# Kernel tuning notes

Measured on AMD Instinct MI355X. Metric: run time of the kernel, lower is better.

The kernel has to match this reference:

```python
import jax, jax.numpy as jnp
import numpy as np

B, C, H, W = 128, 768, 14, 14
D = 128          # d_graph
K = 8            # top_k
LN_EPS = 1e-5
NORM_EPS = 1e-12


def setup_inputs() -> dict:
    key = jax.random.key(0)
    ks = jax.random.split(key, 12)
    s = lambda k, shape, fan: jax.random.normal(k, shape, jnp.float32) / np.sqrt(fan)
    return {
        "feat_map": jax.random.normal(ks[0], (B, C, H, W), jnp.float32),
        # node_proj: Linear(C, D) + LayerNorm(D)
        "W_node": s(ks[1], (C, D), C), "b_node": jnp.zeros((D,), jnp.float32),
        "ln_g": jnp.ones((D,), jnp.float32), "ln_b": jnp.zeros((D,), jnp.float32),
        # pos_mlp: Linear(2, 64) -> GELU -> Linear(64, D)
        "Wp1": s(ks[2], (2, 64), 2), "bp1": jnp.zeros((64,), jnp.float32),
        "Wp2": s(ks[3], (64, D), 64), "bp2": jnp.zeros((D,), jnp.float32),
        # edge_mlp: Linear(3D, D) -> GELU -> Linear(D, D)
        "We1": s(ks[4], (3 * D, D), 3 * D), "be1": jnp.zeros((D,), jnp.float32),
        "We2": s(ks[5], (D, D), D), "be2": jnp.zeros((D,), jnp.float32),
    }


def _layernorm(x, g, b):
    mu = jnp.mean(x, axis=-1, keepdims=True)
    var = jnp.mean(jnp.square(x - mu), axis=-1, keepdims=True)
    return (x - mu) * jax.lax.rsqrt(var + LN_EPS) * g + b


def reference(feat_map, W_node, b_node, ln_g, ln_b, Wp1, bp1, Wp2, bp2, We1, be1, We2, be2):
    Bm, Cm, Hm, Wm = feat_map.shape
    N = Hm * Wm
    tokens = feat_map.reshape(Bm, Cm, N).transpose(0, 2, 1)            # [B,N,C]
    nodes = jax.nn.gelu(_layernorm(tokens @ W_node + b_node, ln_g, ln_b), approximate=False)  # [B,N,D]

    ys = jnp.linspace(0.0, 1.0, Hm)
    xs = jnp.linspace(0.0, 1.0, Wm)
    gy, gx = jnp.meshgrid(ys, xs, indexing='ij')
    coords = jnp.stack([gy.reshape(-1), gx.reshape(-1)], axis=-1)       # [N,2]
    coords = jnp.broadcast_to(coords[None], (Bm, N, 2))

    nrm = nodes / jnp.maximum(jnp.linalg.norm(nodes, axis=-1, keepdims=True), NORM_EPS)
    sim = jnp.einsum('bnd,bmd->bnm', nrm, nrm)
    sim = sim - jnp.eye(N, dtype=sim.dtype)[None] * 1e9
    _, adj = jax.lax.top_k(sim, K)                                      # [B,N,K]

    adj_flat = adj.reshape(Bm, N * K, 1)
    neighbor_nodes = jnp.take_along_axis(nodes, adj_flat, axis=1).reshape(Bm, N, K, -1)
    neighbor_coords = jnp.take_along_axis(coords, adj_flat, axis=1).reshape(Bm, N, K, 2)

    disp = neighbor_coords - coords[:, :, None, :]                      # [B,N,K,2]
    spatial_feat = jax.nn.gelu(disp @ Wp1 + bp1, approximate=False) @ Wp2 + bp2  # [B,N,K,D]

    source = jnp.broadcast_to(nodes[:, :, None, :], neighbor_nodes.shape)
    edge_input = jnp.concatenate([source, neighbor_nodes, spatial_feat], axis=-1)  # [B,N,K,3D]
    edges = jax.nn.gelu(edge_input @ We1 + be1, approximate=False) @ We2 + be2
    return nodes, edges, adj
```

## Files before the change

kernel.cpp:

```cpp
#include <hip/hip_runtime.h>

#define BB 128
#define CC 768
#define NN 196
#define DD 128
#define KTOP 8
#define MROWS 25088

typedef unsigned short u16;
typedef unsigned int u32;

typedef __attribute__((ext_vector_type(8))) short bf16x8;
typedef __attribute__((ext_vector_type(4))) float f32x4;

__device__ __forceinline__ u16 f2bfu(float x) {
    u32 i; __builtin_memcpy(&i, &x, 4);
    u32 r = (i + 0x7fffu + ((i >> 16) & 1u)) >> 16;
    return (u16)r;
}
__device__ __forceinline__ float bfu2f(u16 h) {
    u32 x = ((u32)h) << 16; float f; __builtin_memcpy(&f, &x, 4); return f;
}
__device__ __forceinline__ float gelu_f(float x) {
    return 0.5f * x * (1.0f + erff(x * 0.70710678118654752f));
}

__global__ __launch_bounds__(256)
void pack_we1_kernel(const float* __restrict__ We1, uint4* __restrict__ WPH,
                     uint4* __restrict__ WPL)
{
    const int eid = blockIdx.x * 256 + threadIdx.x;
    const int mat = eid >> 11, rem = eid & 2047;
    const int kc = rem >> 9, ct = (rem >> 6) & 7, l = rem & 63;
    const int g = l >> 4, c = ct * 16 + (l & 15);
    const int krow = mat * 128 + kc * 32 + g * 8;
    u32 h[4], lo[4];
#pragma unroll
    for (int jp = 0; jp < 4; ++jp) {
        const float w0 = We1[(size_t)(krow + 2 * jp) * DD + c];
        const float w1 = We1[(size_t)(krow + 2 * jp + 1) * DD + c];
        const u16 h0 = f2bfu(w0), h1 = f2bfu(w1);
        const u16 l0 = f2bfu(w0 - bfu2f(h0)), l1 = f2bfu(w1 - bfu2f(h1));
        h[jp]  = (u32)h0 | ((u32)h1 << 16);
        lo[jp] = (u32)l0 | ((u32)l1 << 16);
    }
    WPH[eid] = make_uint4(h[0], h[1], h[2], h[3]);
    WPL[eid] = make_uint4(lo[0], lo[1], lo[2], lo[3]);
}

__global__ __launch_bounds__(128)
void gemm_node_kernel(const float* __restrict__ feat, const float* __restrict__ Wn,
                      float* __restrict__ part)
{
    __shared__ float As[32][32];
    __shared__ float Bs[32][DD];
    const int tid = threadIdx.x;
    const int m0  = blockIdx.x * 32;
    const int k0  = blockIdx.y * 384;

    const int r_ld   = tid & 31;
    const int cl_ld  = tid >> 5;
    const int m_ld   = m0 + r_ld;
    const int b_ld   = m_ld / NN;
    const int n_ld   = m_ld % NN;
    const float* fbase = feat + (size_t)b_ld * CC * NN + n_ld;

    const int rg = tid >> 5;
    const int cg = tid & 31;

    float acc[8][4];
#pragma unroll
    for (int i = 0; i < 8; ++i)
#pragma unroll
        for (int j = 0; j < 4; ++j) acc[i][j] = 0.0f;

    for (int kt = 0; kt < 12; ++kt) {
        const int kbase = k0 + kt * 32;
#pragma unroll
        for (int p = 0; p < 8; ++p) {
            const int cl = cl_ld + 4 * p;
            As[cl][r_ld] = fbase[(size_t)(kbase + cl) * NN];
        }
#pragma unroll
        for (int p = 0; p < 8; ++p) {
            const int q = tid + 128 * p;
            const int cl = q >> 5, d4 = (q & 31) * 4;
            *(float4*)(&Bs[cl][d4]) = *(const float4*)(&Wn[(size_t)(kbase + cl) * DD + d4]);
        }
        __syncthreads();
#pragma unroll
        for (int kk = 0; kk < 32; ++kk) {
            const float4 a0 = *(const float4*)(&As[kk][rg * 8]);
            const float4 a1 = *(const float4*)(&As[kk][rg * 8 + 4]);
            const float4 bv = *(const float4*)(&Bs[kk][cg * 4]);
            const float af[8] = {a0.x, a0.y, a0.z, a0.w, a1.x, a1.y, a1.z, a1.w};
#pragma unroll
            for (int i = 0; i < 8; ++i) {
                acc[i][0] += af[i] * bv.x; acc[i][1] += af[i] * bv.y;
                acc[i][2] += af[i] * bv.z; acc[i][3] += af[i] * bv.w;
            }
        }
        __syncthreads();
    }
    float* op = part + ((size_t)blockIdx.y * MROWS + m0 + rg * 8) * DD + cg * 4;
#pragma unroll
    for (int i = 0; i < 8; ++i) {
        *(float4*)(op + (size_t)i * DD) =
            make_float4(acc[i][0], acc[i][1], acc[i][2], acc[i][3]);
    }
}

__global__ __launch_bounds__(128)
void ln_kernel(const float* __restrict__ part, const float* __restrict__ bnode,
               const float* __restrict__ lng, const float* __restrict__ lnb,
               float* __restrict__ nodes, float* __restrict__ inv_norm)
{
    __shared__ float vals[8][DD];
    __shared__ float stats[8][2];
    const int tid = threadIdx.x;
    const int row0 = blockIdx.x * 8;
    const int d = tid;
    const float bb = bnode[d];
#pragma unroll
    for (int r = 0; r < 8; ++r) {
        const size_t m = row0 + r;
        vals[r][d] = part[m * DD + d] + part[(size_t)(MROWS + m) * DD + d] + bb;
    }
    __syncthreads();
    const int lane = tid & 63, wv = tid >> 6;
    for (int r = wv * 4; r < wv * 4 + 4; ++r) {
        float a0 = vals[r][lane], a1 = vals[r][lane + 64];
        float s = a0 + a1;
#pragma unroll
        for (int off = 32; off > 0; off >>= 1) s += __shfl_xor(s, off);
        const float mu = s * (1.0f / 128.0f);
        float d0 = a0 - mu, d1 = a1 - mu;
        float s2 = d0 * d0 + d1 * d1;
#pragma unroll
        for (int off = 32; off > 0; off >>= 1) s2 += __shfl_xor(s2, off);
        if (lane == 0) { stats[r][0] = mu; stats[r][1] = rsqrtf(s2 * (1.0f/128.0f) + 1e-5f); }
    }
    __syncthreads();
    const float g  = lng[d];
    const float be = lnb[d];
    float acc[8];
#pragma unroll
    for (int r = 0; r < 8; ++r) {
        const float y = (vals[r][d] - stats[r][0]) * stats[r][1] * g + be;
        acc[r] = gelu_f(y);
    }
    __syncthreads();
#pragma unroll
    for (int r = 0; r < 8; ++r) vals[r][d] = acc[r] * acc[r];
#pragma unroll
    for (int r = 0; r < 8; ++r) nodes[(size_t)(row0 + r) * DD + d] = acc[r];
    __syncthreads();
    for (int r = wv * 4; r < wv * 4 + 4; ++r) {
        float s = vals[r][lane] + vals[r][lane + 64];
#pragma unroll
        for (int off = 32; off > 0; off >>= 1) s += __shfl_xor(s, off);
        if (lane == 0) inv_norm[row0 + r] = 1.0f / fmaxf(sqrtf(s), 1e-12f);
    }
}

__global__ __launch_bounds__(256)
void s1n1_kernel(const float* __restrict__ nodes, const uint4* __restrict__ WPH,
                 const uint4* __restrict__ WPL, float* __restrict__ S1,
                 float* __restrict__ N1)
{
    __shared__ uint4 AfH[4][4][64];
    __shared__ uint4 AfL[4][4][64];
    const int tid = threadIdx.x;
    const int m0 = blockIdx.x * 64;

#pragma unroll
    for (int p = 0; p < 8; ++p) {
        const int idx = tid + 256 * p;
        const int r = idx >> 5, d0 = (idx & 31) * 4;
        const float4 v = *(const float4*)(&nodes[(size_t)(m0 + r) * DD + d0]);
        const u16 h0 = f2bfu(v.x), h1 = f2bfu(v.y), h2 = f2bfu(v.z), h3 = f2bfu(v.w);
        const u16 l0 = f2bfu(v.x - bfu2f(h0)), l1 = f2bfu(v.y - bfu2f(h1));
        const u16 l2 = f2bfu(v.z - bfu2f(h2)), l3 = f2bfu(v.w - bfu2f(h3));
        const int rt = r >> 4, kc = d0 >> 5;
        const int ln = (((d0 >> 3) & 3) << 4) | (r & 15);
        const int half = (d0 >> 2) & 1;
        u32* ph = (u32*)&AfH[rt][kc][ln];
        u32* pl = (u32*)&AfL[rt][kc][ln];
        ph[half * 2]     = (u32)h0 | ((u32)h1 << 16);
        ph[half * 2 + 1] = (u32)h2 | ((u32)h3 << 16);
        pl[half * 2]     = (u32)l0 | ((u32)l1 << 16);
        pl[half * 2 + 1] = (u32)l2 | ((u32)l3 << 16);
    }
    __syncthreads();

    const int l  = tid & 63;
    const int wv = tid >> 6;
    const int wr = wv >> 1, wc = wv & 1;

    f32x4 acc[2][8];
#pragma unroll
    for (int rt = 0; rt < 2; ++rt)
#pragma unroll
        for (int ct = 0; ct < 8; ++ct) {
            f32x4 z = {0.0f, 0.0f, 0.0f, 0.0f};
            acc[rt][ct] = z;
        }

#pragma unroll
    for (int kc = 0; kc < 4; ++kc) {
        bf16x8 aH[2], aL[2];
#pragma unroll
        for (int rt = 0; rt < 2; ++rt) {
            const uint4 uh = AfH[wr * 2 + rt][kc][l];
            const uint4 ul = AfL[wr * 2 + rt][kc][l];
            __builtin_memcpy(&aH[rt], &uh, 16);
            __builtin_memcpy(&aL[rt], &ul, 16);
        }
#pragma unroll
        for (int ct = 0; ct < 8; ++ct) {
            const uint4 uh = WPH[((wc * 4 + kc) * 8 + ct) * 64 + l];
            const uint4 ul = WPL[((wc * 4 + kc) * 8 + ct) * 64 + l];
            bf16x8 bH, bL;
            __builtin_memcpy(&bH, &uh, 16);
            __builtin_memcpy(&bL, &ul, 16);
#pragma unroll
            for (int rt = 0; rt < 2; ++rt) {
                acc[rt][ct] = __builtin_amdgcn_mfma_f32_16x16x32_bf16(aH[rt], bH, acc[rt][ct], 0, 0, 0);
                acc[rt][ct] = __builtin_amdgcn_mfma_f32_16x16x32_bf16(aL[rt], bH, acc[rt][ct], 0, 0, 0);
                acc[rt][ct] = __builtin_amdgcn_mfma_f32_16x16x32_bf16(aH[rt], bL, acc[rt][ct], 0, 0, 0);
            }
        }
    }

    float* outb = wc ? N1 : S1;
    const int cl  = l & 15;
    const int rq0 = (l >> 4) * 4;
#pragma unroll
    for (int rt = 0; rt < 2; ++rt)
#pragma unroll
        for (int q = 0; q < 4; ++q) {
            const size_t row = m0 + wr * 32 + rt * 16 + rq0 + q;
#pragma unroll
            for (int ct = 0; ct < 8; ++ct)
                outb[row * DD + ct * 16 + cl] = acc[rt][ct][q];
        }
}

__global__ __launch_bounds__(256)
void sim_kernel(const float* __restrict__ nodes, const float* __restrict__ inv_norm,
                float* __restrict__ sim)
{
    __shared__ float as[28][36];
    __shared__ float bs[NN][36];
    __shared__ float invs[NN];
    const int tid = threadIdx.x;
    const int b  = blockIdx.x / 7;
    const int n0 = (blockIdx.x % 7) * 28;
    const float* nb = nodes + (size_t)b * NN * DD;
    if (tid < NN) invs[tid] = inv_norm[b * NN + tid];
    const bool act = tid < 196;
    const int ai = act ? tid / 28 : 0;
    const int bi = act ? tid % 28 : 0;
    float acc[4][7];
#pragma unroll
    for (int r = 0; r < 4; ++r)
#pragma unroll
        for (int j = 0; j < 7; ++j) acc[r][j] = 0.0f;
    for (int dc = 0; dc < DD; dc += 32) {
        __syncthreads();
        if (tid < 224) {
            const int i = tid >> 3, q = tid & 7;
            *(float4*)(&as[i][q * 4]) = *(const float4*)(&nb[(size_t)(n0 + i) * DD + dc + q * 4]);
        }
        for (int idx = tid; idx < 1568; idx += 256) {
            const int r = idx >> 3, q = idx & 7;
            *(float4*)(&bs[r][q * 4]) = *(const float4*)(&nb[(size_t)r * DD + dc + q * 4]);
        }
        __syncthreads();
        if (act) {
            for (int dd = 0; dd < 32; dd += 4) {
                float4 a4[4], b4[7];
#pragma unroll
                for (int r = 0; r < 4; ++r) a4[r] = *(const float4*)(&as[ai * 4 + r][dd]);
#pragma unroll
                for (int j = 0; j < 7; ++j) b4[j] = *(const float4*)(&bs[bi * 7 + j][dd]);
#pragma unroll
                for (int r = 0; r < 4; ++r)
#pragma unroll
                    for (int j = 0; j < 7; ++j)
                        acc[r][j] += a4[r].x * b4[j].x + a4[r].y * b4[j].y
                                   + a4[r].z * b4[j].z + a4[r].w * b4[j].w;
            }
        }
    }
    if (act) {
#pragma unroll
        for (int r = 0; r < 4; ++r) {
            const int n = n0 + ai * 4 + r;
            const float sn = invs[n];
#pragma unroll
            for (int j = 0; j < 7; ++j) {
                const int m = bi * 7 + j;
                sim[((size_t)b * NN + n) * NN + m] = acc[r][j] * sn * invs[m];
            }
        }
    }
}

__global__ __launch_bounds__(256)
void topk_kernel(const float* __restrict__ sim, int* __restrict__ adj_i,
                 float* __restrict__ adj_o, const float* __restrict__ We2,
                 uint4* __restrict__ W2P)
{
    const int bid = blockIdx.x;
    if (bid >= (BB * NN) / 4) {
        const int e  = (bid - (BB * NN) / 4) * 256 + threadIdx.x;
        const int l  = e & 63;
        const int fi = e >> 6;
        const int ks = fi >> 3, ct = fi & 7;
        const int k0 = ks * 32 + (l >> 4) * 8;
        const int c  = ct * 16 + (l & 15);
        u16 v[8];
#pragma unroll
        for (int j = 0; j < 8; ++j) v[j] = f2bfu(We2[(size_t)(k0 + j) * DD + c]);
        uint4 pk;
        pk.x = (u32)v[0] | ((u32)v[1] << 16);
        pk.y = (u32)v[2] | ((u32)v[3] << 16);
        pk.z = (u32)v[4] | ((u32)v[5] << 16);
        pk.w = (u32)v[6] | ((u32)v[7] << 16);
        W2P[e] = pk;
        return;
    }
    const int bn = bid * 4 + (threadIdx.x >> 6);
    const int n = bn % NN;
    const int lane = threadIdx.x & 63;
    const float* srow = sim + (size_t)bn * NN;
    float v[4]; int mi[4];
#pragma unroll
    for (int s = 0; s < 4; ++s) {
        const int m = lane + 64 * s;
        mi[s] = m;
        v[s] = (m < NN && m != n) ? srow[m] : -3.0e38f;
    }
    for (int r = 0; r < KTOP; ++r) {
        float bv = v[0]; int bm = mi[0];
#pragma unroll
        for (int s = 1; s < 4; ++s) { if (v[s] > bv) { bv = v[s]; bm = mi[s]; } }
#pragma unroll
        for (int off = 32; off > 0; off >>= 1) {
            const float ov = __shfl_xor(bv, off);
            const int   om = __shfl_xor(bm, off);
            if (ov > bv || (ov == bv && om < bm)) { bv = ov; bm = om; }
        }
        if (lane == 0) {
            adj_i[bn * KTOP + r] = bm;
            adj_o[bn * KTOP + r] = (float)bm;
        }
#pragma unroll
        for (int s = 0; s < 4; ++s) if (mi[s] == bm) v[s] = -3.0e38f;
    }
}

__global__ __launch_bounds__(128)
void pos_kernel(const float* __restrict__ Wp1, const float* __restrict__ bp1,
                const float* __restrict__ Wp2, const float* __restrict__ bp2,
                const float* __restrict__ We1, float* __restrict__ PC)
{
    __shared__ float t1[64];
    __shared__ float sp[DD];
    const int e = blockIdx.x;
    const int dy = e / 27 - 13, dx = e % 27 - 13;
    const float fy = (float)dy / 13.0f, fx = (float)dx / 13.0f;
    const int tid = threadIdx.x;
    if (tid < 64) {
        const float h = fy * Wp1[tid] + fx * Wp1[64 + tid] + bp1[tid];
        t1[tid] = gelu_f(h);
    }
    __syncthreads();
    float s = bp2[tid];
    for (int j = 0; j < 64; ++j) s += t1[j] * Wp2[j * DD + tid];
    sp[tid] = s;
    __syncthreads();
    float o = 0.0f;
    for (int c = 0; c < DD; ++c) o += sp[c] * We1[(size_t)(256 + c) * DD + tid];
    PC[e * DD + tid] = o;
}

__global__ __launch_bounds__(256)
void edge_kernel(const float* __restrict__ S1, const float* __restrict__ N1,
                 const float* __restrict__ PC, const int* __restrict__ adj_i,
                 const float* __restrict__ be1, const uint4* __restrict__ W2P,
                 const float* __restrict__ be2, float* __restrict__ edges_o)
{
    __shared__ uint4 ldsB[2048];
    const int tid = threadIdx.x;
    const int b  = blockIdx.x / 25;
    const int n0 = (blockIdx.x % 25) * 8;

#pragma unroll
    for (int p = 0; p < 8; ++p)
        ldsB[tid + 256 * p] = W2P[tid + 256 * p];

    const int l  = tid & 63;
    const int wv = tid >> 6;
    const int g  = l >> 4;
    const int rA = wv * 16 + (l & 15);
    const int nA0 = n0 + (rA >> 3);
    const int nA  = (nA0 < NN) ? nA0 : 0;
    const int kA  = rA & 7;
    const int m   = adj_i[((size_t)b * NN + nA) * KTOP + kA];
    const int iy = nA / 14, ix = nA % 14;
    const int my = m / 14,  mx = m % 14;
    const int di = (my - iy + 13) * 27 + (mx - ix + 13);

    const float* s1r = S1 + ((size_t)b * NN + nA) * DD;
    const float* n1r = N1 + ((size_t)b * NN + m) * DD;
    const float* pcr = PC + (size_t)di * DD;

    bf16x8 afr[4];
#pragma unroll
    for (int ks = 0; ks < 4; ++ks) {
        const int k0 = ks * 32 + g * 8;
        float u[8];
#pragma unroll
        for (int h = 0; h < 2; ++h) {
            const int k = k0 + h * 4;
            const float4 s1 = *(const float4*)(s1r + k);
            const float4 n1 = *(const float4*)(n1r + k);
            const float4 pc = *(const float4*)(pcr + k);
            const float4 b1 = *(const float4*)(be1 + k);
            u[h * 4 + 0] = gelu_f(s1.x + n1.x + pc.x + b1.x);
            u[h * 4 + 1] = gelu_f(s1.y + n1.y + pc.y + b1.y);
            u[h * 4 + 2] = gelu_f(s1.z + n1.z + pc.z + b1.z);
            u[h * 4 + 3] = gelu_f(s1.w + n1.w + pc.w + b1.w);
        }
        bf16x8 a;
#pragma unroll
        for (int j = 0; j < 8; ++j) a[j] = (short)f2bfu(u[j]);
        afr[ks] = a;
    }
    __syncthreads();

    f32x4 acc[8];
#pragma unroll
    for (int ct = 0; ct < 8; ++ct) {
        f32x4 z = {0.0f, 0.0f, 0.0f, 0.0f};
        acc[ct] = z;
    }
#pragma unroll
    for (int ks = 0; ks < 4; ++ks) {
#pragma unroll
        for (int ct = 0; ct < 8; ++ct) {
            const uint4 bw = ldsB[(ks * 8 + ct) * 64 + l];
            bf16x8 bf; __builtin_memcpy(&bf, &bw, 16);
            acc[ct] = __builtin_amdgcn_mfma_f32_16x16x32_bf16(afr[ks], bf, acc[ct], 0, 0, 0);
        }
    }

    const int cl  = l & 15;
    const int rq0 = (l >> 4) * 4;
    float be2f[8];
#pragma unroll
    for (int ct = 0; ct < 8; ++ct) be2f[ct] = be2[ct * 16 + cl];
#pragma unroll
    for (int q = 0; q < 4; ++q) {
        const int r = wv * 16 + rq0 + q;
        const int n = n0 + (r >> 3);
        if (n < NN) {
            float* op = edges_o + (((size_t)b * NN + n) * KTOP + (r & 7)) * DD;
#pragma unroll
            for (int ct = 0; ct < 8; ++ct)
                op[ct * 16 + cl] = acc[ct][q] + be2f[ct];
        }
    }
}

extern "C" void kernel_launch(void* const* d_in, const int* in_sizes, int n_in,
                              void* d_out, int out_size, void* d_ws, size_t ws_size,
                              hipStream_t stream)
{
    const float* feat = (const float*)d_in[0];
    const float* Wn   = (const float*)d_in[1];
    const float* bn   = (const float*)d_in[2];
    const float* lng  = (const float*)d_in[3];
    const float* lnb  = (const float*)d_in[4];
    const float* Wp1  = (const float*)d_in[5];
    const float* bp1  = (const float*)d_in[6];
    const float* Wp2  = (const float*)d_in[7];
    const float* bp2  = (const float*)d_in[8];
    const float* We1  = (const float*)d_in[9];
    const float* be1  = (const float*)d_in[10];
    const float* We2  = (const float*)d_in[11];
    const float* be2  = (const float*)d_in[12];

    float* ws = (float*)d_ws;
    float* part     = ws;
    float* sim      = ws;
    float* S1       = ws + 4917248;
    float* N1       = ws + 8128512;
    float* PC       = ws + 11339776;
    float* inv_norm = ws + 11433088;
    int*   adj_i    = (int*)(ws + 11458176);
    uint4* W2P      = (uint4*)(ws + 11433088);
    uint4* WPH      = (uint4*)(ws + 11339776);
    uint4* WPL      = WPH + 4096;

    float* out      = (float*)d_out;
    float* nodes    = out;
    float* edges_o  = out + 3211264;
    float* adj_o    = out + 3211264 + 25690112;

    pack_we1_kernel<<<16, 256, 0, stream>>>(We1, WPH, WPL);
    gemm_node_kernel<<<dim3(784, 2), 128, 0, stream>>>(feat, Wn, part);
    ln_kernel<<<3136, 128, 0, stream>>>(part, bn, lng, lnb, nodes, inv_norm);
    s1n1_kernel<<<392, 256, 0, stream>>>(nodes, WPH, WPL, S1, N1);
    pos_kernel<<<729, 128, 0, stream>>>(Wp1, bp1, Wp2, bp2, We1, PC);
    sim_kernel<<<BB * 7, 256, 0, stream>>>(nodes, inv_norm, sim);
    topk_kernel<<<(BB * NN) / 4 + 8, 256, 0, stream>>>(sim, adj_i, adj_o, We2, W2P);
    edge_kernel<<<BB * 25, 256, 0, stream>>>(S1, N1, PC, adj_i, be1, W2P, be2, edges_o);
}
```

Measured before the change: 392.4 us.

## Double-buffer node GEMM tiles with direct global-to-LDS async loads

The node-projection GEMM now stages its A and B tiles straight into shared memory with global_load_lds, and uses two buffers so the next K-tile loads while the current one is computed. This removes the register round-trip for tile loads and hides global load latency behind the FMA loop. It doubles LDS use per block, which may lower occupancy, and relies on the lane-to-LDS address mapping of the async loads matching the old tile layout.

Result: slower. 400.7 us (+2.1%).

```diff
diff --git a/kernel.cpp b/kernel.cpp
--- a/kernel.cpp
+++ b/kernel.cpp
@@ -12,6 +12,9 @@
 
 typedef __attribute__((ext_vector_type(8))) short bf16x8;
 typedef __attribute__((ext_vector_type(4))) float f32x4;
+
+#define GLDS4(gp, lp)  __builtin_amdgcn_global_load_lds((const __attribute__((address_space(1))) void*)(gp), (__attribute__((address_space(3))) void*)(lp), 4, 0, 0)
+#define GLDS16(gp, lp) __builtin_amdgcn_global_load_lds((const __attribute__((address_space(1))) void*)(gp), (__attribute__((address_space(3))) void*)(lp), 16, 0, 0)
 
 __device__ __forceinline__ u16 f2bfu(float x) {
     u32 i; __builtin_memcpy(&i, &x, 4);
@@ -52,8 +55,8 @@
 void gemm_node_kernel(const float* __restrict__ feat, const float* __restrict__ Wn,
                       float* __restrict__ part)
 {
-    __shared__ float As[32][32];
-    __shared__ float Bs[32][DD];
+    __shared__ float As[2][32][32];
+    __shared__ float Bs[2][32][DD];
     const int tid = threadIdx.x;
     const int m0  = blockIdx.x * 32;
     const int k0  = blockIdx.y * 384;
@@ -65,6 +68,7 @@
     const int n_ld   = m_ld % NN;
     const float* fbase = feat + (size_t)b_ld * CC * NN + n_ld;
 
+    const int wv = tid >> 6;
     const int rg = tid >> 5;
     const int cg = tid & 31;
 
@@ -74,25 +78,32 @@
 #pragma unroll
         for (int j = 0; j < 4; ++j) acc[i][j] = 0.0f;
 
-    for (int kt = 0; kt < 12; ++kt) {
-        const int kbase = k0 + kt * 32;
-#pragma unroll
-        for (int p = 0; p < 8; ++p) {
-            const int cl = cl_ld + 4 * p;
-            As[cl][r_ld] = fbase[(size_t)(kbase + cl) * NN];
-        }
+    auto stage = [&](int buf, int kbase) {
+#pragma unroll
+        for (int p = 0; p < 8; ++p)
+            GLDS4(fbase + (size_t)(kbase + cl_ld + 4 * p) * NN,
+                  &As[buf][wv * 2 + 4 * p][0]);
 #pragma unroll
         for (int p = 0; p < 8; ++p) {
             const int q = tid + 128 * p;
             const int cl = q >> 5, d4 = (q & 31) * 4;
-            *(float4*)(&Bs[cl][d4]) = *(const float4*)(&Wn[(size_t)(kbase + cl) * DD + d4]);
-        }
-        __syncthreads();
+            GLDS16(&Wn[(size_t)(kbase + cl) * DD + d4],
+                   (float*)Bs[buf] + wv * 256 + p * 512);
+        }
+    };
+
+    stage(0, k0);
+    asm volatile("s_waitcnt vmcnt(0)" ::: "memory");
+    __syncthreads();
+
+    int cur = 0;
+    for (int kt = 0; kt < 12; ++kt) {
+        if (kt < 11) stage(cur ^ 1, k0 + (kt + 1) * 32);
 #pragma unroll
         for (int kk = 0; kk < 32; ++kk) {
-            const float4 a0 = *(const float4*)(&As[kk][rg * 8]);
-            const float4 a1 = *(const float4*)(&As[kk][rg * 8 + 4]);
-            const float4 bv = *(const float4*)(&Bs[kk][cg * 4]);
+            const float4 a0 = *(const float4*)(&As[cur][kk][rg * 8]);
+            const float4 a1 = *(const float4*)(&As[cur][kk][rg * 8 + 4]);
+            const float4 bv = *(const float4*)(&Bs[cur][kk][cg * 4]);
             const float af[8] = {a0.x, a0.y, a0.z, a0.w, a1.x, a1.y, a1.z, a1.w};
 #pragma unroll
             for (int i = 0; i < 8; ++i) {
@@ -100,7 +111,9 @@
                 acc[i][2] += af[i] * bv.z; acc[i][3] += af[i] * bv.w;
             }
         }
+        asm volatile("s_waitcnt vmcnt(0)" ::: "memory");
         __syncthreads();
+        cur ^= 1;
     }
     float* op = part + ((size_t)blockIdx.y * MROWS + m0 + rg * 8) * DD + cg * 4;
 #pragma unroll
```
